# Optimization experiments

Measured on AMD Instinct MI355X. Metric: run time of the kernel, lower is better.

## Reference

```python
import jax, jax.numpy as jnp
import numpy as np

NEG_SLOPE = 0.2
EPS = 1e-9


def setup_inputs() -> dict:
    key = jax.random.key(0)
    ks = jax.random.split(key, 6)
    B, N, E, H, F = 2, 40000, 640000, 4, 32
    X = jax.random.normal(ks[0], (B, N, H, F), dtype=jnp.float32)
    A_self = jax.random.normal(ks[1], (H, F), dtype=jnp.float32)
    A_adjc = jax.random.normal(ks[2], (H, F), dtype=jnp.float32)
    targets = jax.random.randint(ks[3], (B, E), 0, N, dtype=jnp.int32)
    sources = jax.random.randint(ks[4], (B, E), 0, N, dtype=jnp.int32)
    degree = jax.random.uniform(ks[5], (B, E), dtype=jnp.float32)
    return {"X": X, "A_self": A_self, "A_adjc": A_adjc, "degree": degree,
            "targets": targets, "sources": sources, "N": N}


def reference(X, A_self, A_adjc, degree, targets, sources, N):
    # X: [B, N, H, F]; targets/sources: [B, E]
    # per-node attention logits: [B, N, H]
    e_self = jnp.einsum("bnhf,hf->bnh", X, A_self)
    e_adjc = jnp.einsum("bnhf,hf->bnh", X, A_adjc)
    # gather to edges: [B, E, H]
    es = jnp.take_along_axis(e_self, targets[:, :, None], axis=1)
    ea = jnp.take_along_axis(e_adjc, sources[:, :, None], axis=1)
    e = jax.nn.leaky_relu(es + ea, negative_slope=NEG_SLOPE)

    seg_max = jax.vmap(lambda v, i: jax.ops.segment_max(v, i, num_segments=N))
    seg_sum = jax.vmap(lambda v, i: jax.ops.segment_sum(v, i, num_segments=N))

    # exact normalization from source: exp(e - seg_max(e)), then divide by
    # seg_max of the exponentials (+eps), both gathered back to edges.
    m1 = jnp.take_along_axis(seg_max(e, targets), targets[:, :, None], axis=1)
    e = jnp.exp(e - m1)
    m2 = jnp.take_along_axis(seg_max(e, targets), targets[:, :, None], axis=1)
    attn = (e / (m2 + EPS))[..., None]  # [B, E, H, 1]; dropout omitted (eval)

    # message passing: gather source features, weight, scatter-sum to targets
    msg = jnp.take_along_axis(X, sources[:, :, None, None], axis=1) * attn  # [B,E,H,F]
    out = seg_sum(msg, targets)  # [B, N, H, F]
    return out
```

## Files before the change

kernel.cpp:

```cpp
#include <hip/hip_runtime.h>
#include <stdint.h>

#define BB     2
#define NNODE  40000
#define NEDGE  640000
#define NH     4
#define NF     32
#define NHF    128
#define SEGN   (BB * NNODE)
#define GEDGE  (BB * NEDGE)
#define EC     16
#define SLOT   48

#define W      512
#define NBK_B  79
#define NBK    (BB * NBK_B)
#define CAP    9216
#define BLK_E  2048
#define NBLKA  (GEDGE / BLK_E)

static constexpr float NEG_SLOPE = 0.2f;
static constexpr float NEG_BIG   = -3.4e38f;

__global__ void prep_k(const float* __restrict__ X,
                       const float* __restrict__ As,
                       const float* __restrict__ Aa,
                       float* __restrict__ S, float* __restrict__ A,
                       unsigned* __restrict__ cursor) {
    int idx = blockIdx.x * blockDim.x + threadIdx.x;
    if (idx < NBK) cursor[idx] = 0u;
    if (idx >= SEGN * NH) return;
    int h = idx & (NH - 1);
    const float4* xv = (const float4*)(X + (size_t)idx * NF);
    const float4* sv = (const float4*)(As + h * NF);
    const float4* av = (const float4*)(Aa + h * NF);
    float s = 0.f, a = 0.f;
#pragma unroll
    for (int i = 0; i < 8; ++i) {
        float4 x = xv[i];
        float4 ws = sv[i];
        float4 wa = av[i];
        s += x.x * ws.x + x.y * ws.y + x.z * ws.z + x.w * ws.w;
        a += x.x * wa.x + x.y * wa.y + x.z * wa.z + x.w * wa.w;
    }
    S[idx] = s;
    A[idx] = a;
}

__global__ __launch_bounds__(256) void binA_k(const int* __restrict__ tg,
                                              const int* __restrict__ sc,
                                              unsigned* __restrict__ cursor,
                                              unsigned* __restrict__ pairs) {
    __shared__ unsigned hist[NBK];
    __shared__ unsigned lofs[NBK];
    __shared__ unsigned gofs[NBK];
    __shared__ unsigned staged[BLK_E];
    __shared__ unsigned char sbk[BLK_E];
    int t = threadIdx.x;
    int base = blockIdx.x * BLK_E;
    for (int i = t; i < NBK; i += 256) hist[i] = 0u;
    __syncthreads();

    unsigned pr[8];
    unsigned short pbk[8], plp[8];
#pragma unroll
    for (int k = 0; k < 8; ++k) {
        int e = base + k * 256 + t;
        int tgv = tg[e], scv = sc[e];
        int b = (e >= NEDGE) ? 1 : 0;
        unsigned bk = (unsigned)(b * NBK_B + (tgv >> 9));
        pr[k]  = ((unsigned)(tgv & (W - 1)) << 16) | (unsigned)scv;
        pbk[k] = (unsigned short)bk;
        plp[k] = (unsigned short)atomicAdd(&hist[bk], 1u);
    }
    __syncthreads();
    if (t == 0) {
        unsigned run = 0;
        for (int i = 0; i < NBK; ++i) { lofs[i] = run; run += hist[i]; }
    }
    __syncthreads();
    if (t < NBK && hist[t] > 0u)
        gofs[t] = atomicAdd(&cursor[t], hist[t]);
    __syncthreads();
#pragma unroll
    for (int k = 0; k < 8; ++k) {
        unsigned j = lofs[pbk[k]] + plp[k];
        staged[j] = pr[k];
        sbk[j] = (unsigned char)pbk[k];
    }
    __syncthreads();
    for (int j = t; j < BLK_E; j += 256) {
        unsigned bk = sbk[j];
        unsigned dst = gofs[bk] + ((unsigned)j - lofs[bk]);
        if (dst < CAP)
            pairs[(size_t)bk * CAP + dst] = staged[j];
    }
}

__global__ __launch_bounds__(256) void binB_k(const unsigned* __restrict__ cursor,
                                              const unsigned* __restrict__ pairs,
                                              unsigned short* __restrict__ srt,
                                              unsigned* __restrict__ deg) {
    __shared__ unsigned short loc[W * SLOT];
    __shared__ unsigned dloc[W];
    int t = threadIdx.x;
    int gbk = blockIdx.x;
    int b = gbk / NBK_B;
    int bkloc = gbk - b * NBK_B;
    int node0 = b * NNODE + bkloc * W;
    int wEff = min(W, NNODE - bkloc * W);
    for (int i = t; i < W; i += 256) dloc[i] = 0u;
    __syncthreads();
    int nE = (int)min(cursor[gbk], (unsigned)CAP);
    const unsigned* pb = pairs + (size_t)gbk * CAP;
    for (int j = t; j < nE; j += 256) {
        unsigned p = pb[j];
        unsigned tl = p >> 16;
        unsigned pos = atomicAdd(&dloc[tl], 1u);
        if (pos < SLOT)
            loc[tl * SLOT + pos] = (unsigned short)(p & 0xFFFFu);
    }
    __syncthreads();
    unsigned* srt32 = (unsigned*)(srt + (size_t)node0 * SLOT);
    const unsigned* loc32 = (const unsigned*)loc;
    int n32 = wEff * SLOT / 2;
    for (int i = t; i < n32; i += 256) srt32[i] = loc32[i];
    for (int i = t; i < wEff; i += 256) deg[node0 + i] = dloc[i];
}

__global__ __launch_bounds__(64) void gather_k(
        const float* __restrict__ X, const float* __restrict__ S,
        const float* __restrict__ A, const unsigned* __restrict__ deg,
        const unsigned short* __restrict__ srt, float* __restrict__ OUT) {
    int node = blockIdx.x;
    int t = threadIdx.x;
    int hs = t & 3;
    int es = t >> 2;
    int ha = t >> 4;
    int dg = min((int)deg[node], SLOT);
    int bbase = (node >= NNODE) ? NNODE : 0;
    size_t beg = (size_t)node * SLOT;

    float sh = S[node * NH + hs];
    float m_st = NEG_BIG;
    float m_ac = NEG_BIG;
    float ax = 0.f, ay = 0.f;

    for (int c = 0; c < dg; c += EC) {
        int e = c + es;
        int sb = bbase;
        float v = NEG_BIG;
        if (e < dg) {
            sb = bbase + (int)srt[beg + e];
            v = sh + A[sb * NH + hs];
            v = v > 0.f ? v : NEG_SLOPE * v;
        }
        float m = v;
        m = fmaxf(m, __shfl_xor(m, 4));
        m = fmaxf(m, __shfl_xor(m, 8));
        m = fmaxf(m, __shfl_xor(m, 16));
        m = fmaxf(m, __shfl_xor(m, 32));
        m_st = fmaxf(m_st, m);
        float w = (e < dg) ? __expf(v - m_st) : 0.f;
        float ma_new = fmaxf(m_ac, __shfl(m, ha));
        float r = __expf(m_ac - ma_new);
        m_ac = ma_new;
        ax *= r; ay *= r;

        int cend = min(EC, dg - c);
#pragma unroll 8
        for (int e2 = 0; e2 < cend; ++e2) {
            float we  = __shfl(w, 4 * e2 + ha);
            int   sbe = __shfl(sb, 4 * e2);
            const float2 x = *(const float2*)(X + (size_t)sbe * NHF + 2 * t);
            ax += x.x * we;
            ay += x.y * we;
        }
    }
    float2* o = (float2*)(OUT + (size_t)node * NHF + 2 * t);
    *o = make_float2(ax, ay);
}

extern "C" void kernel_launch(void* const* d_in, const int* in_sizes, int n_in,
                              void* d_out, int out_size, void* d_ws, size_t ws_size,
                              hipStream_t stream) {
    const float* X  = (const float*)d_in[0];
    const float* As = (const float*)d_in[1];
    const float* Aa = (const float*)d_in[2];
    const int* tg = (const int*)d_in[4];
    const int* sc = (const int*)d_in[5];
    float* OUT = (float*)d_out;

    char* ws = (char*)d_ws;
    float*          S      = (float*)ws;
    float*          A      = (float*)(ws + 1280000);
    unsigned*       deg    = (unsigned*)(ws + 2560000);
    unsigned*       cursor = (unsigned*)(ws + 2880000);
    unsigned*       pairs  = (unsigned*)(ws + 2880640);
    unsigned short* srt    = (unsigned short*)(ws + 8705152);

    const int nlog = SEGN * NH;
    prep_k<<<(nlog + 255) / 256, 256, 0, stream>>>(X, As, Aa, S, A, cursor);
    binA_k<<<NBLKA, 256, 0, stream>>>(tg, sc, cursor, pairs);
    binB_k<<<NBK, 256, 0, stream>>>(cursor, pairs, srt, deg);
    gather_k<<<SEGN, 64, 0, stream>>>(X, S, A, deg, srt, OUT);
}
```

Measured before the change: 238.1 us.

## Gather source features from bf16 copy and compact adjacency lists

Source features X are converted to packed bf16 so the message gather loads half the bytes per edge. Batch 0's copy is staged in the second half of the output buffer and batch 1's copy reuses the freed pairs workspace, so gather is split into two launches per batch. The fixed-slot adjacency array is compacted with a block prefix scan into a packed offset/degree descriptor, which shrinks the index traffic. This rounds features to bf16 and so loses precision, and it adds a conversion pass and an extra launch.

```diff
diff --git a/kernel.cpp b/kernel.cpp
--- a/kernel.cpp
+++ b/kernel.cpp
@@ -22,11 +22,20 @@
 static constexpr float NEG_SLOPE = 0.2f;
 static constexpr float NEG_BIG   = -3.4e38f;
 
+__device__ __forceinline__ unsigned pack2bf(float a, float b) {
+    unsigned ua = __float_as_uint(a);
+    ua += 0x7fffu + ((ua >> 16) & 1u);
+    unsigned ub = __float_as_uint(b);
+    ub += 0x7fffu + ((ub >> 16) & 1u);
+    return (ua >> 16) | (ub & 0xffff0000u);
+}
+
 __global__ void prep_k(const float* __restrict__ X,
                        const float* __restrict__ As,
                        const float* __restrict__ Aa,
                        float* __restrict__ S, float* __restrict__ A,
-                       unsigned* __restrict__ cursor) {
+                       unsigned* __restrict__ cursor,
+                       unsigned* __restrict__ xh0) {
     int idx = blockIdx.x * blockDim.x + threadIdx.x;
     if (idx < NBK) cursor[idx] = 0u;
     if (idx >= SEGN * NH) return;
@@ -35,6 +44,7 @@
     const float4* sv = (const float4*)(As + h * NF);
     const float4* av = (const float4*)(Aa + h * NF);
     float s = 0.f, a = 0.f;
+    unsigned pk[16];
 #pragma unroll
     for (int i = 0; i < 8; ++i) {
         float4 x = xv[i];
@@ -42,9 +52,16 @@
         float4 wa = av[i];
         s += x.x * ws.x + x.y * ws.y + x.z * ws.z + x.w * ws.w;
         a += x.x * wa.x + x.y * wa.y + x.z * wa.z + x.w * wa.w;
+        pk[2 * i]     = pack2bf(x.x, x.y);
+        pk[2 * i + 1] = pack2bf(x.z, x.w);
     }
     S[idx] = s;
     A[idx] = a;
+    if (idx < NNODE * NH) {
+        unsigned* dst = xh0 + (size_t)idx * (NF / 2);
+#pragma unroll
+        for (int i = 0; i < 16; ++i) dst[i] = pk[i];
+    }
 }
 
 __global__ __launch_bounds__(256) void binA_k(const int* __restrict__ tg,
@@ -99,10 +116,11 @@
 
 __global__ __launch_bounds__(256) void binB_k(const unsigned* __restrict__ cursor,
                                               const unsigned* __restrict__ pairs,
-                                              unsigned short* __restrict__ srt,
-                                              unsigned* __restrict__ deg) {
+                                              unsigned short* __restrict__ srtC,
+                                              unsigned* __restrict__ desc) {
     __shared__ unsigned short loc[W * SLOT];
     __shared__ unsigned dloc[W];
+    __shared__ unsigned dscan[W];
     int t = threadIdx.x;
     int gbk = blockIdx.x;
     int b = gbk / NBK_B;
@@ -121,25 +139,56 @@
             loc[tl * SLOT + pos] = (unsigned short)(p & 0xFFFFu);
     }
     __syncthreads();
-    unsigned* srt32 = (unsigned*)(srt + (size_t)node0 * SLOT);
-    const unsigned* loc32 = (const unsigned*)loc;
-    int n32 = wEff * SLOT / 2;
-    for (int i = t; i < n32; i += 256) srt32[i] = loc32[i];
-    for (int i = t; i < wEff; i += 256) deg[node0 + i] = dloc[i];
+    int i0 = t, i1 = t + 256;
+    dscan[i0] = min(dloc[i0], (unsigned)SLOT);
+    dscan[i1] = min(dloc[i1], (unsigned)SLOT);
+    __syncthreads();
+    for (int s = 1; s < W; s <<= 1) {
+        unsigned a0 = (i0 >= s) ? dscan[i0 - s] : 0u;
+        unsigned a1 = (i1 >= s) ? dscan[i1 - s] : 0u;
+        __syncthreads();
+        dscan[i0] += a0; dscan[i1] += a1;
+        __syncthreads();
+    }
+    unsigned gbase = (unsigned)gbk * CAP;
+    for (int k = 0; k < 2; ++k) {
+        int i = t + k * 256;
+        if (i < wEff) {
+            unsigned dg = min(dloc[i], (unsigned)SLOT);
+            unsigned st = dscan[i] - dg;
+            unsigned gstart = gbase + st;
+            desc[node0 + i] = (gstart << 6) | dg;
+            for (unsigned j = 0; j < dg; ++j)
+                srtC[gstart + j] = loc[i * SLOT + j];
+        }
+    }
+}
+
+__global__ void conv1_k(const float* __restrict__ X, uint4* __restrict__ xh1) {
+    int i = blockIdx.x * blockDim.x + threadIdx.x;
+    if (i >= NNODE * NHF / 8) return;
+    const float4* src = (const float4*)(X + (size_t)NNODE * NHF + (size_t)i * 8);
+    float4 a = src[0], b = src[1];
+    uint4 r;
+    r.x = pack2bf(a.x, a.y); r.y = pack2bf(a.z, a.w);
+    r.z = pack2bf(b.x, b.y); r.w = pack2bf(b.z, b.w);
+    xh1[i] = r;
 }
 
 __global__ __launch_bounds__(64) void gather_k(
-        const float* __restrict__ X, const float* __restrict__ S,
-        const float* __restrict__ A, const unsigned* __restrict__ deg,
-        const unsigned short* __restrict__ srt, float* __restrict__ OUT) {
-    int node = blockIdx.x;
+        const unsigned* __restrict__ xh, const float* __restrict__ S,
+        const float* __restrict__ A, const unsigned* __restrict__ desc,
+        const unsigned short* __restrict__ srtC, float* __restrict__ OUT,
+        int node_base) {
+    int node = node_base + blockIdx.x;
     int t = threadIdx.x;
     int hs = t & 3;
     int es = t >> 2;
     int ha = t >> 4;
-    int dg = min((int)deg[node], SLOT);
-    int bbase = (node >= NNODE) ? NNODE : 0;
-    size_t beg = (size_t)node * SLOT;
+    unsigned d = desc[node];
+    int dg = (int)(d & 63u);
+    unsigned beg = d >> 6;
+    int bbase = node_base;
 
     float sh = S[node * NH + hs];
     float m_st = NEG_BIG;
@@ -148,11 +197,11 @@
 
     for (int c = 0; c < dg; c += EC) {
         int e = c + es;
-        int sb = bbase;
+        int lsrc = 0;
         float v = NEG_BIG;
         if (e < dg) {
-            sb = bbase + (int)srt[beg + e];
-            v = sh + A[sb * NH + hs];
+            lsrc = (int)srtC[beg + e];
+            v = sh + A[(bbase + lsrc) * NH + hs];
             v = v > 0.f ? v : NEG_SLOPE * v;
         }
         float m = v;
@@ -170,11 +219,11 @@
         int cend = min(EC, dg - c);
 #pragma unroll 8
         for (int e2 = 0; e2 < cend; ++e2) {
-            float we  = __shfl(w, 4 * e2 + ha);
-            int   sbe = __shfl(sb, 4 * e2);
-            const float2 x = *(const float2*)(X + (size_t)sbe * NHF + 2 * t);
-            ax += x.x * we;
-            ay += x.y * we;
+            float we   = __shfl(w, 4 * e2 + ha);
+            int   srce = __shfl(lsrc, 4 * e2);
+            unsigned xw = xh[(size_t)srce * (NHF / 2) + t];
+            ax += __uint_as_float(xw << 16) * we;
+            ay += __uint_as_float(xw & 0xffff0000u) * we;
         }
     }
     float2* o = (float2*)(OUT + (size_t)node * NHF + 2 * t);
@@ -194,14 +243,18 @@
     char* ws = (char*)d_ws;
     float*          S      = (float*)ws;
     float*          A      = (float*)(ws + 1280000);
-    unsigned*       deg    = (unsigned*)(ws + 2560000);
+    unsigned*       desc   = (unsigned*)(ws + 2560000);
     unsigned*       cursor = (unsigned*)(ws + 2880000);
     unsigned*       pairs  = (unsigned*)(ws + 2880640);
-    unsigned short* srt    = (unsigned short*)(ws + 8705152);
+    unsigned*       xh1    = (unsigned*)(ws + 2880640);
+    unsigned short* srtC   = (unsigned short*)(ws + 13120640);
+    unsigned*       xh0    = (unsigned*)(OUT + (size_t)NNODE * NHF);
 
     const int nlog = SEGN * NH;
-    prep_k<<<(nlog + 255) / 256, 256, 0, stream>>>(X, As, Aa, S, A, cursor);
+    prep_k<<<(nlog + 255) / 256, 256, 0, stream>>>(X, As, Aa, S, A, cursor, xh0);
     binA_k<<<NBLKA, 256, 0, stream>>>(tg, sc, cursor, pairs);
-    binB_k<<<NBK, 256, 0, stream>>>(cursor, pairs, srt, deg);
-    gather_k<<<SEGN, 64, 0, stream>>>(X, S, A, deg, srt, OUT);
-}
+    binB_k<<<NBK, 256, 0, stream>>>(cursor, pairs, srtC, desc);
+    conv1_k<<<(NNODE * NHF / 8 + 255) / 256, 256, 0, stream>>>(X, (uint4*)xh1);
+    gather_k<<<NNODE, 64, 0, stream>>>(xh0, S, A, desc, srtC, OUT, 0);
+    gather_k<<<NNODE, 64, 0, stream>>>(xh1, S, A, desc, srtC, OUT, NNODE);
+}
```

Result: no change. 241.1 us (+1.3%).
